# Kernel tuning notes

Measured on AMD Instinct MI355X. Metric: run time of the kernel, lower is better.

## Reference

```python
import jax, jax.numpy as jnp
import numpy as np

W_L1, W_NORMAL, W_LAPLACIAN = 1.0, 1.0, 0.1
NORM_EPS = 1e-6   # F.normalize eps
COS_EPS = 1e-8    # F.cosine_similarity default eps


def setup_inputs() -> dict:
    key = jax.random.key(0)
    k1, k2, k3, k4, k5, k6 = jax.random.split(key, 6)
    N, F, NNZ = 1_000_000, 2_000_000, 8_000_000
    return {
        "V_rec": jax.random.normal(k1, (N, 3), dtype=jnp.float32),
        "V_gt": jax.random.normal(k2, (N, 3), dtype=jnp.float32),
        "faces": jax.random.randint(k3, (F, 3), 0, N, dtype=jnp.int64)
        if jax.config.jax_enable_x64 else jax.random.randint(k3, (F, 3), 0, N, dtype=jnp.int32),
        "L_rows": jax.random.randint(k4, (NNZ,), 0, N, dtype=jnp.int32),
        "L_cols": jax.random.randint(k5, (NNZ,), 0, N, dtype=jnp.int32),
        "L_vals": jax.random.normal(k6, (NNZ,), dtype=jnp.float32),
    }


def _vertex_normals(verts, faces):
    # gather verts by face indices: [F,3] each
    v0 = verts[faces[:, 0]]
    v1 = verts[faces[:, 1]]
    v2 = verts[faces[:, 2]]
    face_normals = jnp.cross(v1 - v0, v2 - v0)  # [F,3]
    vn = (jnp.zeros_like(verts)
          .at[faces[:, 0]].add(face_normals)
          .at[faces[:, 1]].add(face_normals)
          .at[faces[:, 2]].add(face_normals))
    norm = jnp.linalg.norm(vn, axis=1, keepdims=True)
    return vn / jnp.maximum(norm, NORM_EPS)


def _cosine_sim(a, b):
    dot = jnp.sum(a * b, axis=1)
    na = jnp.linalg.norm(a, axis=1)
    nb = jnp.linalg.norm(b, axis=1)
    return dot / (jnp.maximum(na, COS_EPS) * jnp.maximum(nb, COS_EPS))


def _spmm(rows, cols, vals, V):
    # sparse [N,N] @ dense [N,3] via gather + segment_sum
    return jax.ops.segment_sum(vals[:, None] * V[cols], rows, num_segments=V.shape[0])


def reference(V_rec, V_gt, faces, L_rows, L_cols, L_vals):
    # L1 term
    loss_l1 = jnp.mean(jnp.abs(V_rec - V_gt))
    # Normal cosine term
    normals_gt = _vertex_normals(V_gt, faces)
    normals_rec = _vertex_normals(V_rec, faces)
    cos_n = jnp.nan_to_num(_cosine_sim(normals_rec, normals_gt), nan=1.0)
    loss_normal = jnp.mean(1.0 - cos_n)
    # Laplacian cosine term
    delta_gt = _spmm(L_rows, L_cols, L_vals, V_gt)
    delta_rec = _spmm(L_rows, L_cols, L_vals, V_rec)
    cos_l = jnp.nan_to_num(_cosine_sim(delta_rec, delta_gt), nan=1.0)
    loss_laplacian = jnp.mean(1.0 - cos_l)
    finite = jnp.isfinite(delta_gt).all() & jnp.isfinite(delta_rec).all()
    loss_laplacian = jnp.where(finite, loss_laplacian, 0.0)
    return W_L1 * loss_l1 + W_NORMAL * loss_normal + W_LAPLACIAN * loss_laplacian
```

## Files before the change

kernel.cpp:

```cpp
#include <hip/hip_runtime.h>
#include <hip/hip_bf16.h>

#define NORM_EPS_F 1e-6f
#define COS_EPS_F  1e-8f
#define BK   512
#define BKSH 9
#define NBGMAX 2048

__device__ __forceinline__ void atomAddF(float* p, float v) {
    unsafeAtomicAdd(p, v);
}

template<int NV>
__device__ __forceinline__ void blockReduceAtomicN(float (&v)[NV], float* dst) {
    #pragma unroll
    for (int off = 32; off > 0; off >>= 1) {
        #pragma unroll
        for (int k = 0; k < NV; ++k) v[k] += __shfl_down(v[k], off, 64);
    }
    __shared__ float red[4][NV];
    int wave = threadIdx.x >> 6, lane = threadIdx.x & 63;
    if (lane == 0) {
        #pragma unroll
        for (int k = 0; k < NV; ++k) red[wave][k] = v[k];
    }
    __syncthreads();
    if (threadIdx.x == 0) {
        float s[NV];
        #pragma unroll
        for (int k = 0; k < NV; ++k) s[k] = 0.f;
        for (int w = 0; w < 4; ++w)
            #pragma unroll
            for (int k = 0; k < NV; ++k) s[k] += red[w][k];
        #pragma unroll
        for (int k = 0; k < NV; ++k) atomAddF(&dst[k], s[k]);
    }
}


__global__ void __launch_bounds__(256) pack_l1_kernel(
    const float* __restrict__ Vr, const float* __restrict__ Vg,
    float4* __restrict__ Vp, float* __restrict__ accum, int N)
{
    int i = blockIdx.x * blockDim.x + threadIdx.x;
    float l1[1] = {0.f};
    if (i < N) {
        float rx = Vr[3 * i], ry = Vr[3 * i + 1], rz = Vr[3 * i + 2];
        float gx = Vg[3 * i], gy = Vg[3 * i + 1], gz = Vg[3 * i + 2];
        Vp[2 * i]     = make_float4(rx, ry, rz, 0.f);
        Vp[2 * i + 1] = make_float4(gx, gy, gz, 0.f);
        l1[0] = fabsf(rx - gx) + fabsf(ry - gy) + fabsf(rz - gz);
    }
    blockReduceAtomicN<1>(l1, &accum[0]);
}

__global__ void __launch_bounds__(256) fn_kernel(
    const float4* __restrict__ Vp, const int* __restrict__ faces,
    float4* __restrict__ FN, int F)
{
    int half = (F + 1) >> 1;
    int t = blockIdx.x * blockDim.x + threadIdx.x;
    if (t >= half) return;
    int fi[2] = {t, t + half};
    int n = (fi[1] < F) ? 2 : 1;
    int idx[2][3];
    #pragma unroll
    for (int k = 0; k < 2; ++k) {
        if (k < n) {
            idx[k][0] = faces[3 * fi[k]];
            idx[k][1] = faces[3 * fi[k] + 1];
            idx[k][2] = faces[3 * fi[k] + 2];
        }
    }
    float4 r0[2], r1[2], r2[2], g0[2], g1[2], g2[2];
    #pragma unroll
    for (int k = 0; k < 2; ++k) {
        if (k < n) {
            r0[k] = Vp[2 * idx[k][0]]; g0[k] = Vp[2 * idx[k][0] + 1];
            r1[k] = Vp[2 * idx[k][1]]; g1[k] = Vp[2 * idx[k][1] + 1];
            r2[k] = Vp[2 * idx[k][2]]; g2[k] = Vp[2 * idx[k][2] + 1];
        }
    }
    #pragma unroll
    for (int k = 0; k < 2; ++k) {
        if (k < n) {
            float ax = r1[k].x - r0[k].x, ay = r1[k].y - r0[k].y, az = r1[k].z - r0[k].z;
            float bx = r2[k].x - r0[k].x, by = r2[k].y - r0[k].y, bz = r2[k].z - r0[k].z;
            FN[2 * fi[k]] = make_float4(ay * bz - az * by, az * bx - ax * bz, ax * by - ay * bx, 0.f);
            ax = g1[k].x - g0[k].x; ay = g1[k].y - g0[k].y; az = g1[k].z - g0[k].z;
            bx = g2[k].x - g0[k].x; by = g2[k].y - g0[k].y; bz = g2[k].z - g0[k].z;
            FN[2 * fi[k] + 1] = make_float4(ay * bz - az * by, az * bx - ax * bz, ax * by - ay * bx, 0.f);
        }
    }
}

__global__ void __launch_bounds__(256) bucket_faces_kernel(
    const int* __restrict__ faces, int* __restrict__ cnt,
    unsigned* __restrict__ recF, int capF, int F, int b0, int bcnt, int chunk)
{
    __shared__ int hist[NBGMAX];
    int f0 = blockIdx.x * chunk;
    int f1 = min(f0 + chunk, F);
    for (int b = threadIdx.x; b < bcnt; b += blockDim.x) hist[b] = 0;
    __syncthreads();
    for (int f = f0 + threadIdx.x; f < f1; f += blockDim.x) {
        #pragma unroll
        for (int c = 0; c < 3; ++c) {
            unsigned bb = ((unsigned)faces[3 * f + c] >> BKSH) - (unsigned)b0;
            if (bb < (unsigned)bcnt) atomicAdd(&hist[bb], 1);
        }
    }
    __syncthreads();
    for (int b = threadIdx.x; b < bcnt; b += blockDim.x) {
        int h = hist[b];
        if (h) hist[b] = atomicAdd(&cnt[b], h);
    }
    __syncthreads();
    for (int f = f0 + threadIdx.x; f < f1; f += blockDim.x) {
        #pragma unroll
        for (int c = 0; c < 3; ++c) {
            int vtx = faces[3 * f + c];
            unsigned bb = ((unsigned)vtx >> BKSH) - (unsigned)b0;
            if (bb < (unsigned)bcnt) {
                int pos = atomicAdd(&hist[bb], 1);
                if (pos < capF)
                    recF[(size_t)bb * capF + pos] =
                        ((unsigned)f << BKSH) | (unsigned)(vtx & (BK - 1));
            }
        }
    }
}

__global__ void __launch_bounds__(256) accum_normals_kernel(
    const float4* __restrict__ Vp, const float4* __restrict__ FN,
    const int* __restrict__ faces,
    const int* __restrict__ cnt, const unsigned* __restrict__ recF, int capF,
    float* __restrict__ accum, int N, int b0, int use_fn)
{
    __shared__ float vnr[3 * BK];
    __shared__ float vng[3 * BK];
    int g = blockIdx.x;
    for (int i = threadIdx.x; i < 3 * BK; i += blockDim.x) { vnr[i] = 0.f; vng[i] = 0.f; }
    __syncthreads();

    const unsigned* rec = recF + (size_t)g * capF;
    int n = min(cnt[g], capF);
    int i = threadIdx.x;
    if (use_fn) {
        for (; i + 768 < n; i += 1024) {
            unsigned rc[4];
            rc[0] = rec[i]; rc[1] = rec[i + 256]; rc[2] = rec[i + 512]; rc[3] = rec[i + 768];
            float4 nr[4], ng[4];
            #pragma unroll
            for (int k = 0; k < 4; ++k) {
                int f = rc[k] >> BKSH;
                nr[k] = FN[2 * f];
                ng[k] = FN[2 * f + 1];
            }
            #pragma unroll
            for (int k = 0; k < 4; ++k) {
                int lv = rc[k] & (BK - 1);
                atomicAdd(&vnr[3 * lv + 0], nr[k].x);
                atomicAdd(&vnr[3 * lv + 1], nr[k].y);
                atomicAdd(&vnr[3 * lv + 2], nr[k].z);
                atomicAdd(&vng[3 * lv + 0], ng[k].x);
                atomicAdd(&vng[3 * lv + 1], ng[k].y);
                atomicAdd(&vng[3 * lv + 2], ng[k].z);
            }
        }
    }
    for (; i < n; i += 256) {
        unsigned rc = rec[i];
        int lv = rc & (BK - 1);
        int f  = rc >> BKSH;
        float4 nr, ng;
        if (use_fn) {
            nr = FN[2 * f];
            ng = FN[2 * f + 1];
        } else {
            int i0 = faces[3 * f], i1 = faces[3 * f + 1], i2 = faces[3 * f + 2];
            float4 r0 = Vp[2 * i0], r1 = Vp[2 * i1], r2 = Vp[2 * i2];
            float4 g0 = Vp[2 * i0 + 1], g1 = Vp[2 * i1 + 1], g2 = Vp[2 * i2 + 1];
            float ax = r1.x - r0.x, ay = r1.y - r0.y, az = r1.z - r0.z;
            float bx = r2.x - r0.x, by = r2.y - r0.y, bz = r2.z - r0.z;
            nr = make_float4(ay * bz - az * by, az * bx - ax * bz, ax * by - ay * bx, 0.f);
            ax = g1.x - g0.x; ay = g1.y - g0.y; az = g1.z - g0.z;
            bx = g2.x - g0.x; by = g2.y - g0.y; bz = g2.z - g0.z;
            ng = make_float4(ay * bz - az * by, az * bx - ax * bz, ax * by - ay * bx, 0.f);
        }
        atomicAdd(&vnr[3 * lv + 0], nr.x);
        atomicAdd(&vnr[3 * lv + 1], nr.y);
        atomicAdd(&vnr[3 * lv + 2], nr.z);
        atomicAdd(&vng[3 * lv + 0], ng.x);
        atomicAdd(&vng[3 * lv + 1], ng.y);
        atomicAdd(&vng[3 * lv + 2], ng.z);
    }
    __syncthreads();

    float ln[1] = {0.f};
    for (int lv = threadIdx.x; lv < BK; lv += blockDim.x) {
        int gv = ((b0 + g) << BKSH) + lv;
        if (gv < N) {
            float ax = vnr[3 * lv], ay = vnr[3 * lv + 1], az = vnr[3 * lv + 2];
            float bx = vng[3 * lv], by = vng[3 * lv + 1], bz = vng[3 * lv + 2];
            float na = sqrtf(ax * ax + ay * ay + az * az);
            float nb = sqrtf(bx * bx + by * by + bz * bz);
            float ia = 1.0f / fmaxf(na, NORM_EPS_F);
            float ib = 1.0f / fmaxf(nb, NORM_EPS_F);
            ax *= ia; ay *= ia; az *= ia;
            bx *= ib; by *= ib; bz *= ib;
            float dot = ax * bx + ay * by + az * bz;
            float nna = sqrtf(ax * ax + ay * ay + az * az);
            float nnb = sqrtf(bx * bx + by * by + bz * bz);
            float cosn = dot / (fmaxf(nna, COS_EPS_F) * fmaxf(nnb, COS_EPS_F));
            if (isnan(cosn)) cosn = 1.0f;
            ln[0] += 1.0f - cosn;
        }
    }
    blockReduceAtomicN<1>(ln, &accum[1]);
}

__global__ void __launch_bounds__(256) bucket_L_kernel(
    const int* __restrict__ rows, const int* __restrict__ cols,
    const float* __restrict__ vals, int* __restrict__ cnt,
    int2* __restrict__ recL, int capL, int nnz, int b0, int bcnt, int chunk)
{
    __shared__ int hist[NBGMAX];
    int i0 = blockIdx.x * chunk;
    int i1 = min(i0 + chunk, nnz);
    for (int b = threadIdx.x; b < bcnt; b += blockDim.x) hist[b] = 0;
    __syncthreads();
    for (int i = i0 + threadIdx.x; i < i1; i += blockDim.x) {
        unsigned bb = ((unsigned)rows[i] >> BKSH) - (unsigned)b0;
        if (bb < (unsigned)bcnt) atomicAdd(&hist[bb], 1);
    }
    __syncthreads();
    for (int b = threadIdx.x; b < bcnt; b += blockDim.x) {
        int h = hist[b];
        if (h) hist[b] = atomicAdd(&cnt[b], h);
    }
    __syncthreads();
    for (int i = i0 + threadIdx.x; i < i1; i += blockDim.x) {
        int r = rows[i];
        unsigned bb = ((unsigned)r >> BKSH) - (unsigned)b0;
        if (bb < (unsigned)bcnt) {
            int pos = atomicAdd(&hist[bb], 1);
            if (pos < capL)
                recL[(size_t)bb * capL + pos] = make_int2(
                    (int)(((unsigned)cols[i] << BKSH) | (unsigned)(r & (BK - 1))),
                    __float_as_int(vals[i]));
        }
    }
}

__global__ void __launch_bounds__(256) accum_lap_kernel(
    const float4* __restrict__ Vp,
    const int* __restrict__ cnt, const int2* __restrict__ recL, int capL,
    float* __restrict__ accum, int N, int b0)
{
    __shared__ float dlr[3 * BK];
    __shared__ float dlg[3 * BK];
    int g = blockIdx.x;
    for (int i = threadIdx.x; i < 3 * BK; i += blockDim.x) { dlr[i] = 0.f; dlg[i] = 0.f; }
    __syncthreads();

    const int2* rec = recL + (size_t)g * capL;
    int n = min(cnt[g], capL);
    int i = threadIdx.x;
    for (; i + 768 < n; i += 1024) {
        int2 rc[4];
        rc[0] = rec[i]; rc[1] = rec[i + 256]; rc[2] = rec[i + 512]; rc[3] = rec[i + 768];
        float4 pr[4], pg[4];
        #pragma unroll
        for (int k = 0; k < 4; ++k) {
            int col = (unsigned)rc[k].x >> BKSH;
            pr[k] = Vp[2 * col];
            pg[k] = Vp[2 * col + 1];
        }
        #pragma unroll
        for (int k = 0; k < 4; ++k) {
            int lv = (unsigned)rc[k].x & (BK - 1);
            float v = __int_as_float(rc[k].y);
            atomicAdd(&dlr[3 * lv + 0], v * pr[k].x);
            atomicAdd(&dlr[3 * lv + 1], v * pr[k].y);
            atomicAdd(&dlr[3 * lv + 2], v * pr[k].z);
            atomicAdd(&dlg[3 * lv + 0], v * pg[k].x);
            atomicAdd(&dlg[3 * lv + 1], v * pg[k].y);
            atomicAdd(&dlg[3 * lv + 2], v * pg[k].z);
        }
    }
    for (; i < n; i += 256) {
        int2 rc = rec[i];
        unsigned u = (unsigned)rc.x;
        int lv  = u & (BK - 1);
        int col = u >> BKSH;
        float v = __int_as_float(rc.y);
        float4 pr = Vp[2 * col];
        float4 pg = Vp[2 * col + 1];
        atomicAdd(&dlr[3 * lv + 0], v * pr.x);
        atomicAdd(&dlr[3 * lv + 1], v * pr.y);
        atomicAdd(&dlr[3 * lv + 2], v * pr.z);
        atomicAdd(&dlg[3 * lv + 0], v * pg.x);
        atomicAdd(&dlg[3 * lv + 1], v * pg.y);
        atomicAdd(&dlg[3 * lv + 2], v * pg.z);
    }
    __syncthreads();

    float vals2[2] = {0.f, 0.f};
    for (int lv = threadIdx.x; lv < BK; lv += blockDim.x) {
        int gv = ((b0 + g) << BKSH) + lv;
        if (gv < N) {
            float px = dlr[3 * lv], py = dlr[3 * lv + 1], pz = dlr[3 * lv + 2];
            float qx = dlg[3 * lv], qy = dlg[3 * lv + 1], qz = dlg[3 * lv + 2];
            bool fin = isfinite(px) && isfinite(py) && isfinite(pz) &&
                       isfinite(qx) && isfinite(qy) && isfinite(qz);
            vals2[1] += fin ? 0.f : 1.f;
            float dotl = px * qx + py * qy + pz * qz;
            float npn = sqrtf(px * px + py * py + pz * pz);
            float nqn = sqrtf(qx * qx + qy * qy + qz * qz);
            float cosl = dotl / (fmaxf(npn, COS_EPS_F) * fmaxf(nqn, COS_EPS_F));
            if (isnan(cosl)) cosl = 1.0f;
            vals2[0] += 1.0f - cosl;
        }
    }
    blockReduceAtomicN<2>(vals2, &accum[2]);
}

__global__ void finalize_kernel(const float* __restrict__ accum,
                                float* __restrict__ out, int N)
{
    float invN = 1.0f / (float)N;
    float l1 = accum[0] * invN * (1.0f / 3.0f);
    float ln = accum[1] * invN;
    float ll = (accum[3] > 0.0f) ? 0.0f : accum[2] * invN;
    out[0] = 1.0f * l1 + 1.0f * ln + 0.1f * ll;
}


__global__ void __launch_bounds__(256) face_normals_kernel(
    const float* __restrict__ Vr, const float* __restrict__ Vg,
    const int* __restrict__ faces,
    float* __restrict__ vn_rec, float* __restrict__ vn_gt, int F)
{
    int f = blockIdx.x * blockDim.x + threadIdx.x;
    if (f >= F) return;
    int i0 = faces[3 * f + 0], i1 = faces[3 * f + 1], i2 = faces[3 * f + 2];
    {
        float v0x = Vr[3 * i0], v0y = Vr[3 * i0 + 1], v0z = Vr[3 * i0 + 2];
        float v1x = Vr[3 * i1], v1y = Vr[3 * i1 + 1], v1z = Vr[3 * i1 + 2];
        float v2x = Vr[3 * i2], v2y = Vr[3 * i2 + 1], v2z = Vr[3 * i2 + 2];
        float ax = v1x - v0x, ay = v1y - v0y, az = v1z - v0z;
        float bx = v2x - v0x, by = v2y - v0y, bz = v2z - v0z;
        float nx = ay * bz - az * by, ny = az * bx - ax * bz, nz = ax * by - ay * bx;
        atomAddF(&vn_rec[3 * i0], nx); atomAddF(&vn_rec[3 * i0 + 1], ny); atomAddF(&vn_rec[3 * i0 + 2], nz);
        atomAddF(&vn_rec[3 * i1], nx); atomAddF(&vn_rec[3 * i1 + 1], ny); atomAddF(&vn_rec[3 * i1 + 2], nz);
        atomAddF(&vn_rec[3 * i2], nx); atomAddF(&vn_rec[3 * i2 + 1], ny); atomAddF(&vn_rec[3 * i2 + 2], nz);
    }
    {
        float v0x = Vg[3 * i0], v0y = Vg[3 * i0 + 1], v0z = Vg[3 * i0 + 2];
        float v1x = Vg[3 * i1], v1y = Vg[3 * i1 + 1], v1z = Vg[3 * i1 + 2];
        float v2x = Vg[3 * i2], v2y = Vg[3 * i2 + 1], v2z = Vg[3 * i2 + 2];
        float ax = v1x - v0x, ay = v1y - v0y, az = v1z - v0z;
        float bx = v2x - v0x, by = v2y - v0y, bz = v2z - v0z;
        float nx = ay * bz - az * by, ny = az * bx - ax * bz, nz = ax * by - ay * bx;
        atomAddF(&vn_gt[3 * i0], nx); atomAddF(&vn_gt[3 * i0 + 1], ny); atomAddF(&vn_gt[3 * i0 + 2], nz);
        atomAddF(&vn_gt[3 * i1], nx); atomAddF(&vn_gt[3 * i1 + 1], ny); atomAddF(&vn_gt[3 * i1 + 2], nz);
        atomAddF(&vn_gt[3 * i2], nx); atomAddF(&vn_gt[3 * i2 + 1], ny); atomAddF(&vn_gt[3 * i2 + 2], nz);
    }
}

__global__ void __launch_bounds__(256) spmm_kernel(
    const float* __restrict__ Vr, const float* __restrict__ Vg,
    const int* __restrict__ rows, const int* __restrict__ cols,
    const float* __restrict__ vals,
    float* __restrict__ dl_rec, float* __restrict__ dl_gt, int nnz)
{
    int i = blockIdx.x * blockDim.x + threadIdx.x;
    if (i >= nnz) return;
    int r = rows[i], c = cols[i];
    float v = vals[i];
    atomAddF(&dl_rec[3 * r], v * Vr[3 * c]);
    atomAddF(&dl_rec[3 * r + 1], v * Vr[3 * c + 1]);
    atomAddF(&dl_rec[3 * r + 2], v * Vr[3 * c + 2]);
    atomAddF(&dl_gt[3 * r], v * Vg[3 * c]);
    atomAddF(&dl_gt[3 * r + 1], v * Vg[3 * c + 1]);
    atomAddF(&dl_gt[3 * r + 2], v * Vg[3 * c + 2]);
}

__global__ void __launch_bounds__(256) reduce_kernel(
    const float* __restrict__ Vr, const float* __restrict__ Vg,
    const float* __restrict__ vn_rec, const float* __restrict__ vn_gt,
    const float* __restrict__ dl_rec, const float* __restrict__ dl_gt,
    float* __restrict__ accum, int N)
{
    int i = blockIdx.x * blockDim.x + threadIdx.x;
    float l1 = 0.0f, ln = 0.0f, ll = 0.0f, nonfin = 0.0f;
    if (i < N) {
        float rx = Vr[3 * i], ry = Vr[3 * i + 1], rz = Vr[3 * i + 2];
        float gx = Vg[3 * i], gy = Vg[3 * i + 1], gz = Vg[3 * i + 2];
        l1 = fabsf(rx - gx) + fabsf(ry - gy) + fabsf(rz - gz);
        float ax = vn_rec[3 * i], ay = vn_rec[3 * i + 1], az = vn_rec[3 * i + 2];
        float bx = vn_gt[3 * i],  by = vn_gt[3 * i + 1],  bz = vn_gt[3 * i + 2];
        float na = sqrtf(ax * ax + ay * ay + az * az);
        float nb = sqrtf(bx * bx + by * by + bz * bz);
        float ia = 1.0f / fmaxf(na, NORM_EPS_F);
        float ib = 1.0f / fmaxf(nb, NORM_EPS_F);
        ax *= ia; ay *= ia; az *= ia; bx *= ib; by *= ib; bz *= ib;
        float dot = ax * bx + ay * by + az * bz;
        float nna = sqrtf(ax * ax + ay * ay + az * az);
        float nnb = sqrtf(bx * bx + by * by + bz * bz);
        float cosn = dot / (fmaxf(nna, COS_EPS_F) * fmaxf(nnb, COS_EPS_F));
        if (isnan(cosn)) cosn = 1.0f;
        ln = 1.0f - cosn;
        float px = dl_rec[3 * i], py = dl_rec[3 * i + 1], pz = dl_rec[3 * i + 2];
        float qx = dl_gt[3 * i],  qy = dl_gt[3 * i + 1],  qz = dl_gt[3 * i + 2];
        bool fin = isfinite(px) && isfinite(py) && isfinite(pz) &&
                   isfinite(qx) && isfinite(qy) && isfinite(qz);
        nonfin = fin ? 0.0f : 1.0f;
        float dotl = px * qx + py * qy + pz * qz;
        float npn = sqrtf(px * px + py * py + pz * pz);
        float nqn = sqrtf(qx * qx + qy * qy + qz * qz);
        float cosl = dotl / (fmaxf(npn, COS_EPS_F) * fmaxf(nqn, COS_EPS_F));
        if (isnan(cosl)) cosl = 1.0f;
        ll = 1.0f - cosl;
    }
    float a[1] = {l1};  blockReduceAtomicN<1>(a, &accum[0]);
    float b[1] = {ln};  blockReduceAtomicN<1>(b, &accum[1]);
    float c2[2] = {ll, nonfin}; blockReduceAtomicN<2>(c2, &accum[2]);
}


extern "C" void kernel_launch(void* const* d_in, const int* in_sizes, int n_in,
                              void* d_out, int out_size, void* d_ws, size_t ws_size,
                              hipStream_t stream)
{
    const float* Vr    = (const float*)d_in[0];
    const float* Vg    = (const float*)d_in[1];
    const int*   faces = (const int*)d_in[2];
    const int*   Lr    = (const int*)d_in[3];
    const int*   Lc    = (const int*)d_in[4];
    const float* Lv    = (const float*)d_in[5];

    const int N   = in_sizes[0] / 3;
    const int F   = in_sizes[2] / 3;
    const int NNZ = in_sizes[3];
    const int NB  = (N + BK - 1) >> BKSH;

    float* ws = (float*)d_ws;
    const int B = 256;

    const long long baseW  = 4 + NBGMAX;
    const long long vpackW = 8LL * N;
    const long long fnW    = 8LL * F;
    const long long totW   = (long long)(ws_size / 4);

    const int capF = 3 * F / (NB > 0 ? NB : 1) + 1 + 640;
    const int capL = NNZ / (NB > 0 ? NB : 1) + 1 + 640;

    long long availA = totW - baseW - vpackW - fnW;
    long long availB = totW - baseW - vpackW;
    bool tierA = availA >= (long long)capF * 64;
    long long availF = tierA ? availA : availB;

    int NBG_F = (int)(availF / capF);
    int NBG_L = (int)(availB / (2LL * capL));
    if (NBG_F > NB) NBG_F = NB;
    if (NBG_L > NB) NBG_L = NB;
    if (NBG_F > NBGMAX) NBG_F = NBGMAX;
    if (NBG_L > NBGMAX) NBG_L = NBGMAX;

    bool fast = (N <= (1 << 20)) && (F <= (1 << 22)) &&
                NBG_F >= 32 && NBG_L >= 32;

    if (fast) {
        float*    accum = ws;
        int*      cnt   = (int*)(ws + 4);
        float4*   Vp    = (float4*)(ws + baseW);
        float4*   FN    = (float4*)(ws + baseW + vpackW);
        unsigned* recF  = (unsigned*)(ws + baseW + vpackW + (tierA ? fnW : 0));
        int2*     recL  = (int2*)(ws + baseW + vpackW);

        hipMemsetAsync(accum, 0, 4 * sizeof(float), stream);

        pack_l1_kernel<<<dim3((N + B - 1) / B), dim3(B), 0, stream>>>(Vr, Vg, Vp, accum, N);
        if (tierA) {
            int half = (F + 1) >> 1;
            fn_kernel<<<dim3((half + B - 1) / B), dim3(B), 0, stream>>>(Vp, faces, FN, F);
        }

        const int CHF = 4096, CHL = 8192;
        int passF = (NB + NBG_F - 1) / NBG_F;
        for (int p = 0; p < passF; ++p) {
            int b0 = p * NBG_F;
            int bcnt = NB - b0 < NBG_F ? NB - b0 : NBG_F;
            hipMemsetAsync(cnt, 0, (size_t)bcnt * sizeof(int), stream);
            bucket_faces_kernel<<<dim3((F + CHF - 1) / CHF), dim3(B), 0, stream>>>(
                faces, cnt, recF, capF, F, b0, bcnt, CHF);
            accum_normals_kernel<<<dim3(bcnt), dim3(B), 0, stream>>>(
                Vp, FN, faces, cnt, recF, capF, accum, N, b0, tierA ? 1 : 0);
        }
        int passL = (NB + NBG_L - 1) / NBG_L;
        for (int p = 0; p < passL; ++p) {
            int b0 = p * NBG_L;
            int bcnt = NB - b0 < NBG_L ? NB - b0 : NBG_L;
            hipMemsetAsync(cnt, 0, (size_t)bcnt * sizeof(int), stream);
            bucket_L_kernel<<<dim3((NNZ + CHL - 1) / CHL), dim3(B), 0, stream>>>(
                Lr, Lc, Lv, cnt, recL, capL, NNZ, b0, bcnt, CHL);
            accum_lap_kernel<<<dim3(bcnt), dim3(B), 0, stream>>>(
                Vp, cnt, recL, capL, accum, N, b0);
        }
        finalize_kernel<<<dim3(1), dim3(1), 0, stream>>>(accum, (float*)d_out, N);
    } else {
        float* vn_rec = ws;
        float* vn_gt  = ws + (size_t)3 * N;
        float* dl_rec = ws + (size_t)6 * N;
        float* dl_gt  = ws + (size_t)9 * N;
        float* accum  = ws + (size_t)12 * N;
        hipMemsetAsync(d_ws, 0, ((size_t)12 * N + 4) * sizeof(float), stream);
        face_normals_kernel<<<dim3((F + B - 1) / B), dim3(B), 0, stream>>>(Vr, Vg, faces, vn_rec, vn_gt, F);
        spmm_kernel<<<dim3((NNZ + B - 1) / B), dim3(B), 0, stream>>>(Vr, Vg, Lr, Lc, Lv, dl_rec, dl_gt, NNZ);
        reduce_kernel<<<dim3((N + B - 1) / B), dim3(B), 0, stream>>>(Vr, Vg, vn_rec, vn_gt, dl_rec, dl_gt, accum, N);
        finalize_kernel<<<dim3(1), dim3(1), 0, stream>>>(accum, (float*)d_out, N);
    }
}
```

Baseline: 1.146 ms.

## Replace single-pass bucketing with two-level coarse/fine radix partition

Face and Laplacian records were scattered straight into up to 2048 fine buckets, using a large shared histogram and poorly coalesced scattered writes. They are now first partitioned into at most 64 coarse buckets, each tagged with a byte sub-index, and a second kernel then splits each coarse bucket into 32 fine buckets. The aim is to cut shared-atomic contention and improve write locality. In exchange every record is written and read one extra time, a coarse staging buffer is needed, and workspace sizing changes, which can alter how many passes run.

```diff
diff --git a/kernel.cpp b/kernel.cpp
--- a/kernel.cpp
+++ b/kernel.cpp
@@ -6,6 +6,9 @@
 #define BK   512
 #define BKSH 9
 #define NBGMAX 2048
+#define CHF1 2048
+#define CHL1 4096
+#define K2   32
 
 __device__ __forceinline__ void atomAddF(float* p, float v) {
     unsafeAtomicAdd(p, v);
@@ -65,71 +68,166 @@
     int n = (fi[1] < F) ? 2 : 1;
     int idx[2][3];
     #pragma unroll
-    for (int k = 0; k < 2; ++k) {
-        if (k < n) {
-            idx[k][0] = faces[3 * fi[k]];
-            idx[k][1] = faces[3 * fi[k] + 1];
-            idx[k][2] = faces[3 * fi[k] + 2];
-        }
+    for (int k = 0; k < 2; ++k) if (k < n) {
+        idx[k][0] = faces[3 * fi[k]];
+        idx[k][1] = faces[3 * fi[k] + 1];
+        idx[k][2] = faces[3 * fi[k] + 2];
     }
     float4 r0[2], r1[2], r2[2], g0[2], g1[2], g2[2];
     #pragma unroll
-    for (int k = 0; k < 2; ++k) {
-        if (k < n) {
-            r0[k] = Vp[2 * idx[k][0]]; g0[k] = Vp[2 * idx[k][0] + 1];
-            r1[k] = Vp[2 * idx[k][1]]; g1[k] = Vp[2 * idx[k][1] + 1];
-            r2[k] = Vp[2 * idx[k][2]]; g2[k] = Vp[2 * idx[k][2] + 1];
-        }
+    for (int k = 0; k < 2; ++k) if (k < n) {
+        r0[k] = Vp[2 * idx[k][0]]; g0[k] = Vp[2 * idx[k][0] + 1];
+        r1[k] = Vp[2 * idx[k][1]]; g1[k] = Vp[2 * idx[k][1] + 1];
+        r2[k] = Vp[2 * idx[k][2]]; g2[k] = Vp[2 * idx[k][2] + 1];
     }
     #pragma unroll
-    for (int k = 0; k < 2; ++k) {
-        if (k < n) {
-            float ax = r1[k].x - r0[k].x, ay = r1[k].y - r0[k].y, az = r1[k].z - r0[k].z;
-            float bx = r2[k].x - r0[k].x, by = r2[k].y - r0[k].y, bz = r2[k].z - r0[k].z;
-            FN[2 * fi[k]] = make_float4(ay * bz - az * by, az * bx - ax * bz, ax * by - ay * bx, 0.f);
-            ax = g1[k].x - g0[k].x; ay = g1[k].y - g0[k].y; az = g1[k].z - g0[k].z;
-            bx = g2[k].x - g0[k].x; by = g2[k].y - g0[k].y; bz = g2[k].z - g0[k].z;
-            FN[2 * fi[k] + 1] = make_float4(ay * bz - az * by, az * bx - ax * bz, ax * by - ay * bx, 0.f);
-        }
-    }
-}
-
-__global__ void __launch_bounds__(256) bucket_faces_kernel(
-    const int* __restrict__ faces, int* __restrict__ cnt,
-    unsigned* __restrict__ recF, int capF, int F, int b0, int bcnt, int chunk)
-{
-    __shared__ int hist[NBGMAX];
-    int f0 = blockIdx.x * chunk;
-    int f1 = min(f0 + chunk, F);
-    for (int b = threadIdx.x; b < bcnt; b += blockDim.x) hist[b] = 0;
-    __syncthreads();
-    for (int f = f0 + threadIdx.x; f < f1; f += blockDim.x) {
+    for (int k = 0; k < 2; ++k) if (k < n) {
+        float ax = r1[k].x - r0[k].x, ay = r1[k].y - r0[k].y, az = r1[k].z - r0[k].z;
+        float bx = r2[k].x - r0[k].x, by = r2[k].y - r0[k].y, bz = r2[k].z - r0[k].z;
+        FN[2 * fi[k]] = make_float4(ay * bz - az * by, az * bx - ax * bz, ax * by - ay * bx, 0.f);
+        ax = g1[k].x - g0[k].x; ay = g1[k].y - g0[k].y; az = g1[k].z - g0[k].z;
+        bx = g2[k].x - g0[k].x; by = g2[k].y - g0[k].y; bz = g2[k].z - g0[k].z;
+        FN[2 * fi[k] + 1] = make_float4(ay * bz - az * by, az * bx - ax * bz, ax * by - ay * bx, 0.f);
+    }
+}
+
+
+__global__ void __launch_bounds__(256) bucket_F1(
+    const int* __restrict__ faces, int* __restrict__ cntC,
+    unsigned* __restrict__ recA, unsigned char* __restrict__ recC,
+    int capC, int F, int b0, int bcnt, int chunk)
+{
+    __shared__ int hist[64];
+    int f0 = blockIdx.x * chunk, f1 = min(f0 + chunk, F);
+    if (threadIdx.x < 64) hist[threadIdx.x] = 0;
+    __syncthreads();
+    for (int f = f0 + threadIdx.x; f < f1; f += 256) {
         #pragma unroll
         for (int c = 0; c < 3; ++c) {
-            unsigned bb = ((unsigned)faces[3 * f + c] >> BKSH) - (unsigned)b0;
-            if (bb < (unsigned)bcnt) atomicAdd(&hist[bb], 1);
-        }
-    }
-    __syncthreads();
-    for (int b = threadIdx.x; b < bcnt; b += blockDim.x) {
-        int h = hist[b];
-        if (h) hist[b] = atomicAdd(&cnt[b], h);
-    }
-    __syncthreads();
-    for (int f = f0 + threadIdx.x; f < f1; f += blockDim.x) {
+            unsigned fb = ((unsigned)faces[3 * f + c] >> BKSH) - (unsigned)b0;
+            if (fb < (unsigned)bcnt) atomicAdd(&hist[fb >> 5], 1);
+        }
+    }
+    __syncthreads();
+    if (threadIdx.x < 64) {
+        int h = hist[threadIdx.x];
+        if (h) hist[threadIdx.x] = atomicAdd(&cntC[threadIdx.x], h);
+    }
+    __syncthreads();
+    for (int f = f0 + threadIdx.x; f < f1; f += 256) {
         #pragma unroll
         for (int c = 0; c < 3; ++c) {
-            int vtx = faces[3 * f + c];
-            unsigned bb = ((unsigned)vtx >> BKSH) - (unsigned)b0;
-            if (bb < (unsigned)bcnt) {
-                int pos = atomicAdd(&hist[bb], 1);
-                if (pos < capF)
-                    recF[(size_t)bb * capF + pos] =
-                        ((unsigned)f << BKSH) | (unsigned)(vtx & (BK - 1));
+            int v = faces[3 * f + c];
+            unsigned fb = ((unsigned)v >> BKSH) - (unsigned)b0;
+            if (fb < (unsigned)bcnt) {
+                int pos = atomicAdd(&hist[fb >> 5], 1);
+                if (pos < capC) {
+                    size_t idx = (size_t)(fb >> 5) * capC + pos;
+                    recA[idx] = ((unsigned)f << BKSH) | ((unsigned)v & (BK - 1));
+                    recC[idx] = (unsigned char)(fb & 31);
+                }
             }
         }
     }
 }
+
+__global__ void __launch_bounds__(256) bucket_L1(
+    const int* __restrict__ rows, const int* __restrict__ cols,
+    const float* __restrict__ vals, int* __restrict__ cntC,
+    int2* __restrict__ recA, unsigned char* __restrict__ recC,
+    int capC, int nnz, int b0, int bcnt, int chunk)
+{
+    __shared__ int hist[64];
+    int i0 = blockIdx.x * chunk, i1 = min(i0 + chunk, nnz);
+    if (threadIdx.x < 64) hist[threadIdx.x] = 0;
+    __syncthreads();
+    for (int i = i0 + threadIdx.x; i < i1; i += 256) {
+        unsigned fb = ((unsigned)rows[i] >> BKSH) - (unsigned)b0;
+        if (fb < (unsigned)bcnt) atomicAdd(&hist[fb >> 5], 1);
+    }
+    __syncthreads();
+    if (threadIdx.x < 64) {
+        int h = hist[threadIdx.x];
+        if (h) hist[threadIdx.x] = atomicAdd(&cntC[threadIdx.x], h);
+    }
+    __syncthreads();
+    for (int i = i0 + threadIdx.x; i < i1; i += 256) {
+        int r = rows[i];
+        unsigned fb = ((unsigned)r >> BKSH) - (unsigned)b0;
+        if (fb < (unsigned)bcnt) {
+            int pos = atomicAdd(&hist[fb >> 5], 1);
+            if (pos < capC) {
+                size_t idx = (size_t)(fb >> 5) * capC + pos;
+                recA[idx] = make_int2(
+                    (int)(((unsigned)cols[i] << BKSH) | ((unsigned)r & (BK - 1))),
+                    __float_as_int(vals[i]));
+                recC[idx] = (unsigned char)(fb & 31);
+            }
+        }
+    }
+}
+
+
+__global__ void __launch_bounds__(256) bucket_F2(
+    const int* __restrict__ cntC, const unsigned* __restrict__ recA,
+    const unsigned char* __restrict__ recC, int capC,
+    int* __restrict__ cntFine, unsigned* __restrict__ fine, int capF)
+{
+    __shared__ int hist[32];
+    int c = blockIdx.x;
+    int K = gridDim.y, k = blockIdx.y;
+    int ch = (capC + K - 1) / K;
+    int n = min(cntC[c], capC);
+    int i0 = k * ch, i1 = min(i0 + ch, n);
+    if (threadIdx.x < 32) hist[threadIdx.x] = 0;
+    __syncthreads();
+    const size_t base = (size_t)c * capC;
+    for (int i = i0 + threadIdx.x; i < i1; i += 256)
+        atomicAdd(&hist[recC[base + i]], 1);
+    __syncthreads();
+    if (threadIdx.x < 32) {
+        int h = hist[threadIdx.x];
+        if (h) hist[threadIdx.x] = atomicAdd(&cntFine[(c << 5) + threadIdx.x], h);
+    }
+    __syncthreads();
+    for (int i = i0 + threadIdx.x; i < i1; i += 256) {
+        int fic = recC[base + i];
+        int pos = atomicAdd(&hist[fic], 1);
+        if (pos < capF)
+            fine[(size_t)((c << 5) + fic) * capF + pos] = recA[base + i];
+    }
+}
+
+__global__ void __launch_bounds__(256) bucket_L2(
+    const int* __restrict__ cntC, const int2* __restrict__ recA,
+    const unsigned char* __restrict__ recC, int capC,
+    int* __restrict__ cntFine, int2* __restrict__ fine, int capL)
+{
+    __shared__ int hist[32];
+    int c = blockIdx.x;
+    int K = gridDim.y, k = blockIdx.y;
+    int ch = (capC + K - 1) / K;
+    int n = min(cntC[c], capC);
+    int i0 = k * ch, i1 = min(i0 + ch, n);
+    if (threadIdx.x < 32) hist[threadIdx.x] = 0;
+    __syncthreads();
+    const size_t base = (size_t)c * capC;
+    for (int i = i0 + threadIdx.x; i < i1; i += 256)
+        atomicAdd(&hist[recC[base + i]], 1);
+    __syncthreads();
+    if (threadIdx.x < 32) {
+        int h = hist[threadIdx.x];
+        if (h) hist[threadIdx.x] = atomicAdd(&cntFine[(c << 5) + threadIdx.x], h);
+    }
+    __syncthreads();
+    for (int i = i0 + threadIdx.x; i < i1; i += 256) {
+        int fic = recC[base + i];
+        int pos = atomicAdd(&hist[fic], 1);
+        if (pos < capL)
+            fine[(size_t)((c << 5) + fic) * capL + pos] = recA[base + i];
+    }
+}
+
 
 __global__ void __launch_bounds__(256) accum_normals_kernel(
     const float4* __restrict__ Vp, const float4* __restrict__ FN,
@@ -218,39 +316,6 @@
         }
     }
     blockReduceAtomicN<1>(ln, &accum[1]);
-}
-
-__global__ void __launch_bounds__(256) bucket_L_kernel(
-    const int* __restrict__ rows, const int* __restrict__ cols,
-    const float* __restrict__ vals, int* __restrict__ cnt,
-    int2* __restrict__ recL, int capL, int nnz, int b0, int bcnt, int chunk)
-{
-    __shared__ int hist[NBGMAX];
-    int i0 = blockIdx.x * chunk;
-    int i1 = min(i0 + chunk, nnz);
-    for (int b = threadIdx.x; b < bcnt; b += blockDim.x) hist[b] = 0;
-    __syncthreads();
-    for (int i = i0 + threadIdx.x; i < i1; i += blockDim.x) {
-        unsigned bb = ((unsigned)rows[i] >> BKSH) - (unsigned)b0;
-        if (bb < (unsigned)bcnt) atomicAdd(&hist[bb], 1);
-    }
-    __syncthreads();
-    for (int b = threadIdx.x; b < bcnt; b += blockDim.x) {
-        int h = hist[b];
-        if (h) hist[b] = atomicAdd(&cnt[b], h);
-    }
-    __syncthreads();
-    for (int i = i0 + threadIdx.x; i < i1; i += blockDim.x) {
-        int r = rows[i];
-        unsigned bb = ((unsigned)r >> BKSH) - (unsigned)b0;
-        if (bb < (unsigned)bcnt) {
-            int pos = atomicAdd(&hist[bb], 1);
-            if (pos < capL)
-                recL[(size_t)bb * capL + pos] = make_int2(
-                    (int)(((unsigned)cols[i] << BKSH) | (unsigned)(r & (BK - 1))),
-                    __float_as_int(vals[i]));
-        }
-    }
 }
 
 __global__ void __launch_bounds__(256) accum_lap_kernel(
@@ -449,36 +514,55 @@
     float* ws = (float*)d_ws;
     const int B = 256;
 
-    const long long baseW  = 4 + NBGMAX;
-    const long long vpackW = 8LL * N;
+    const long long totW   = (long long)(ws_size / 4);
+    const long long fixedW = 4 + 64 + NBGMAX;
+    const long long vpW    = 8LL * N;
+    const long long arenaW = totW - fixedW - vpW;
     const long long fnW    = 8LL * F;
-    const long long totW   = (long long)(ws_size / 4);
 
     const int capF = 3 * F / (NB > 0 ? NB : 1) + 1 + 640;
     const int capL = NNZ / (NB > 0 ? NB : 1) + 1 + 640;
 
-    long long availA = totW - baseW - vpackW - fnW;
-    long long availB = totW - baseW - vpackW;
-    bool tierA = availA >= (long long)capF * 64;
-    long long availF = tierA ? availA : availB;
-
-    int NBG_F = (int)(availF / capF);
-    int NBG_L = (int)(availB / (2LL * capL));
-    if (NBG_F > NB) NBG_F = NB;
-    if (NBG_L > NB) NBG_L = NB;
-    if (NBG_F > NBGMAX) NBG_F = NBGMAX;
-    if (NBG_L > NBGMAX) NBG_L = NBGMAX;
+    auto fwords = [&](int nbg) -> long long {
+        long long nc = (nbg + 31) / 32, capC = 32LL * capF;
+        return nc * capC + (nc * capC + 3) / 4 + (long long)nbg * capF + 4;
+    };
+    auto lwords = [&](int nbg) -> long long {
+        long long nc = (nbg + 31) / 32, capC = 32LL * capL;
+        return nc * capC * 2 + (((nc * capC + 3) / 4 + 1) & ~1LL) + (long long)nbg * capL * 2 + 4;
+    };
+
+    int NBG_F = NB < NBGMAX ? NB : NBGMAX;
+    bool tierA = (arenaW - fnW) >= fwords(64);
+    long long arenaF = tierA ? (arenaW - fnW) : arenaW;
+    while (NBG_F > 64 && fwords(NBG_F) > arenaF) NBG_F -= 32;
+    int NBG_L = NB < NBGMAX ? NB : NBGMAX;
+    while (NBG_L > 64 && lwords(NBG_L) > arenaW) NBG_L -= 32;
 
     bool fast = (N <= (1 << 20)) && (F <= (1 << 22)) &&
-                NBG_F >= 32 && NBG_L >= 32;
+                NBG_F >= 64 && NBG_L >= 64 &&
+                fwords(NBG_F) <= arenaF && lwords(NBG_L) <= arenaW &&
+                arenaW > 0;
 
     if (fast) {
-        float*    accum = ws;
-        int*      cnt   = (int*)(ws + 4);
-        float4*   Vp    = (float4*)(ws + baseW);
-        float4*   FN    = (float4*)(ws + baseW + vpackW);
-        unsigned* recF  = (unsigned*)(ws + baseW + vpackW + (tierA ? fnW : 0));
-        int2*     recL  = (int2*)(ws + baseW + vpackW);
+        float*  accum   = ws;
+        int*    cntC    = (int*)(ws + 4);
+        int*    cntFine = (int*)(ws + 68);
+        float4* Vp      = (float4*)(ws + fixedW);
+        float*  arena   = ws + fixedW + vpW;
+
+        const long long NCF = (NBG_F + 31) / 32, capCF = 32LL * capF;
+        float4*        FN    = (float4*)arena;
+        float*         fbase = tierA ? (arena + fnW) : arena;
+        unsigned*      recAF = (unsigned*)fbase;
+        unsigned char* recCF = (unsigned char*)(recAF + NCF * capCF);
+        unsigned*      fineF = (unsigned*)(fbase + NCF * capCF + (NCF * capCF + 3) / 4);
+
+        const long long NCL = (NBG_L + 31) / 32, capCL = 32LL * capL;
+        int2*          recAL = (int2*)arena;
+        unsigned char* recCL = (unsigned char*)(recAL + NCL * capCL);
+        const long long bytesWL = ((NCL * capCL + 3) / 4 + 1) & ~1LL;
+        int2*          fineL = (int2*)(arena + NCL * capCL * 2 + bytesWL);
 
         hipMemsetAsync(accum, 0, 4 * sizeof(float), stream);
 
@@ -488,26 +572,32 @@
             fn_kernel<<<dim3((half + B - 1) / B), dim3(B), 0, stream>>>(Vp, faces, FN, F);
         }
 
-        const int CHF = 4096, CHL = 8192;
         int passF = (NB + NBG_F - 1) / NBG_F;
         for (int p = 0; p < passF; ++p) {
             int b0 = p * NBG_F;
             int bcnt = NB - b0 < NBG_F ? NB - b0 : NBG_F;
-            hipMemsetAsync(cnt, 0, (size_t)bcnt * sizeof(int), stream);
-            bucket_faces_kernel<<<dim3((F + CHF - 1) / CHF), dim3(B), 0, stream>>>(
-                faces, cnt, recF, capF, F, b0, bcnt, CHF);
+            int nc = (bcnt + 31) / 32;
+            hipMemsetAsync(ws + 4, 0, (64 + NBGMAX) * sizeof(int), stream);
+            bucket_F1<<<dim3((F + CHF1 - 1) / CHF1), dim3(B), 0, stream>>>(
+                faces, cntC, recAF, recCF, (int)capCF, F, b0, bcnt, CHF1);
+            bucket_F2<<<dim3(nc, K2), dim3(B), 0, stream>>>(
+                cntC, recAF, recCF, (int)capCF, cntFine, fineF, capF);
             accum_normals_kernel<<<dim3(bcnt), dim3(B), 0, stream>>>(
-                Vp, FN, faces, cnt, recF, capF, accum, N, b0, tierA ? 1 : 0);
-        }
+                Vp, FN, faces, cntFine, fineF, capF, accum, N, b0, tierA ? 1 : 0);
+        }
+
         int passL = (NB + NBG_L - 1) / NBG_L;
         for (int p = 0; p < passL; ++p) {
             int b0 = p * NBG_L;
             int bcnt = NB - b0 < NBG_L ? NB - b0 : NBG_L;
-            hipMemsetAsync(cnt, 0, (size_t)bcnt * sizeof(int), stream);
-            bucket_L_kernel<<<dim3((NNZ + CHL - 1) / CHL), dim3(B), 0, stream>>>(
-                Lr, Lc, Lv, cnt, recL, capL, NNZ, b0, bcnt, CHL);
+            int nc = (bcnt + 31) / 32;
+            hipMemsetAsync(ws + 4, 0, (64 + NBGMAX) * sizeof(int), stream);
+            bucket_L1<<<dim3((NNZ + CHL1 - 1) / CHL1), dim3(B), 0, stream>>>(
+                Lr, Lc, Lv, cntC, recAL, recCL, (int)capCL, NNZ, b0, bcnt, CHL1);
+            bucket_L2<<<dim3(nc, K2), dim3(B), 0, stream>>>(
+                cntC, recAL, recCL, (int)capCL, cntFine, fineL, capL);
             accum_lap_kernel<<<dim3(bcnt), dim3(B), 0, stream>>>(
-                Vp, cnt, recL, capL, accum, N, b0);
+                Vp, cntFine, fineL, capL, accum, N, b0);
         }
         finalize_kernel<<<dim3(1), dim3(1), 0, stream>>>(accum, (float*)d_out, N);
     } else {
```

Measured after the change: 1.098 ms. 4.2% less time.
